# Kernel tuning notes

Hardware: AMD Instinct MI355X
Metric: run time of the kernel (lower is better)

## Reference

```python
import jax, jax.numpy as jnp
import numpy as np

AUDIO_DIM, SEM_DIM, ATTN_DIM = 512, 768, 128


def setup_inputs() -> dict:
    key = jax.random.key(0)
    ks = jax.random.split(key, 12)
    B, T, T_sem = 8, 4096, 1024
    s = lambda d: 1.0 / np.sqrt(d)
    return {
        "x_ct": jax.random.normal(ks[0], (B, AUDIO_DIM, T), jnp.float32),
        "sem_btd": jax.random.normal(ks[1], (B, T_sem, SEM_DIM), jnp.float32),
        "ln_w": jnp.ones((AUDIO_DIM,), jnp.float32),
        "ln_b": jnp.zeros((AUDIO_DIM,), jnp.float32),
        "Wq": jax.random.normal(ks[2], (AUDIO_DIM, ATTN_DIM), jnp.float32) * s(AUDIO_DIM),
        "bq": jnp.zeros((ATTN_DIM,), jnp.float32),
        "Wk": jax.random.normal(ks[3], (SEM_DIM, ATTN_DIM), jnp.float32) * s(SEM_DIM),
        "bk": jnp.zeros((ATTN_DIM,), jnp.float32),
        "Wv": jax.random.normal(ks[4], (SEM_DIM, ATTN_DIM), jnp.float32) * s(SEM_DIM),
        "bv": jnp.zeros((ATTN_DIM,), jnp.float32),
        "Wo": jax.random.normal(ks[5], (ATTN_DIM, AUDIO_DIM), jnp.float32) * s(ATTN_DIM),
        "bo": jnp.zeros((AUDIO_DIM,), jnp.float32),
    }


def _layernorm(x, w, b, eps=1e-5):
    mu = jnp.mean(x, axis=-1, keepdims=True)
    var = jnp.mean(jnp.square(x - mu), axis=-1, keepdims=True)
    return (x - mu) * jax.lax.rsqrt(var + eps) * w + b


def reference(x_ct, sem_btd, ln_w, ln_b, Wq, bq, Wk, bk, Wv, bv, Wo, bo):
    # x_ct: [B, C, T] -> [B, T, C]
    x = jnp.swapaxes(x_ct, 1, 2)
    x = _layernorm(x, ln_w, ln_b)
    Q = x @ Wq + bq                      # [B, T, A]
    K = sem_btd @ Wk + bk                # [B, S, A]
    V = sem_btd @ Wv + bv                # [B, S, A]
    scale = ATTN_DIM ** -0.5
    attn = jnp.einsum("bta,bsa->bts", Q, K) * scale
    attn = jax.nn.softmax(attn, axis=-1)  # dropout: eval mode (identity)
    ctx = jnp.einsum("bts,bsa->bta", attn, V)
    delta = ctx @ Wo + bo                # [B, T, C]
    return jnp.swapaxes(delta, 1, 2)     # [B, C, T]
```

## Files before the change

### kernel.cpp

```cpp
#include <hip/hip_runtime.h>
#include <hip/hip_bf16.h>
#include <math.h>

#define BATCH 8
#define TDIM 4096
#define SDIM 1024
#define CDIM 512
#define DDIM 768
#define ADIM 128

typedef short s8v __attribute__((ext_vector_type(8)));
typedef float f4v __attribute__((ext_vector_type(4)));

__device__ __forceinline__ short f2bf(float f) {
    unsigned u = __float_as_uint(f);
    u += 0x7fffu + ((u >> 16) & 1u);
    return (short)(u >> 16);
}
__device__ __forceinline__ float bf2f(short s) {
    return __uint_as_float(((unsigned)(unsigned short)s) << 16);
}
__device__ __forceinline__ f4v mfma16(s8v a, s8v b, f4v c) {
    return __builtin_amdgcn_mfma_f32_16x16x32_bf16(a, b, c, 0, 0, 0);
}

__global__ __launch_bounds__(256) void prep_w(
    const float* __restrict__ Wq, const float* __restrict__ Wk,
    const float* __restrict__ Wv, const float* __restrict__ Wo,
    const float* __restrict__ lnw, const float* __restrict__ lnb,
    short* __restrict__ WqT, short* __restrict__ WkT,
    short* __restrict__ WvT, short* __restrict__ WoT,
    float* __restrict__ uv)
{
    int tid = threadIdx.x;
    int gid = blockIdx.x * 256 + tid;
    {
        int k = gid >> 7, n = gid & 127;
        WqT[n * 512 + k] = f2bf(Wq[gid] * lnw[k]);
    }
    #pragma unroll
    for (int i = 0; i < 2; ++i) {
        int e = gid + i * 65536;
        if (e < 98304) {
            int k = e >> 7, n = e & 127;
            WkT[n * 768 + k] = f2bf(Wk[e]);
            WvT[n * 768 + k] = f2bf(Wv[e]);
        }
    }
    {
        int k = gid >> 9, c = gid & 511;
        WoT[c * 128 + k] = f2bf(Wo[gid]);
    }
    if (blockIdx.x < 32) {
        int a = tid & 127, half = tid >> 7;
        float pu = 0.f, pv = 0.f;
        #pragma unroll
        for (int cc = 0; cc < 8; ++cc) {
            int c = blockIdx.x * 16 + half * 8 + cc;
            float wq = Wq[c * 128 + a];
            pu += lnb[c] * wq;
            pv += lnw[c] * wq;
        }
        atomicAdd(&uv[a], pu);
        atomicAdd(&uv[128 + a], pv);
    }
}

__global__ __launch_bounds__(256) void kv_proj(
    const float* __restrict__ sem,
    const short* __restrict__ WkT, const float* __restrict__ bk,
    const short* __restrict__ WvT, const float* __restrict__ bv,
    short* __restrict__ Kb, short* __restrict__ Vb)
{
    __shared__ __align__(16) short sA[32 * 40];
    __shared__ __align__(16) short sW[2][128 * 40];
    const int tid = threadIdx.x, lane = tid & 63, wave = tid >> 6;
    const int ln15 = lane & 15, q = lane >> 4, kq = q * 8;
    const int r0 = blockIdx.x * 32;
    const int b = r0 >> 10, sbase = r0 & 1023;
    const int kv = wave >> 1;
    const int mh = wave & 1;
    const int m  = mh * 16 + ln15;

    f4v acc[8];
    #pragma unroll
    for (int j = 0; j < 8; ++j) acc[j] = (f4v)0.0f;

    const int srow = tid >> 3;
    const int sk4  = (tid & 7) * 4;

    for (int kc = 0; kc < DDIM / 32; ++kc) {
        __syncthreads();
        {
            float4 f = *(const float4*)&sem[(size_t)(r0 + srow) * DDIM + kc * 32 + sk4];
            uint2 pk;
            pk.x = (unsigned short)f2bf(f.x) | ((unsigned)(unsigned short)f2bf(f.y) << 16);
            pk.y = (unsigned short)f2bf(f.z) | ((unsigned)(unsigned short)f2bf(f.w) << 16);
            *(uint2*)&sA[srow * 40 + sk4] = pk;
        }
        #pragma unroll
        for (int i = 0; i < 2; ++i) {
            int idx8 = i * 256 + tid;
            int n = idx8 >> 2, k8 = (idx8 & 3) * 8;
            *(s8v*)&sW[0][n * 40 + k8] = *(const s8v*)&WkT[(size_t)n * 768 + kc * 32 + k8];
            *(s8v*)&sW[1][n * 40 + k8] = *(const s8v*)&WvT[(size_t)n * 768 + kc * 32 + k8];
        }
        __syncthreads();
        s8v a = *(const s8v*)&sA[m * 40 + kq];
        #pragma unroll
        for (int j = 0; j < 8; ++j) {
            s8v bb = *(const s8v*)&sW[kv][(j * 16 + ln15) * 40 + kq];
            acc[j] = mfma16(a, bb, acc[j]);
        }
    }
    const int s_in_b = sbase + mh * 16 + q * 4;
    if (kv == 0) {
        #pragma unroll
        for (int j = 0; j < 8; ++j) {
            int col = j * 16 + ln15;
            float bias = bk[col];
            #pragma unroll
            for (int r = 0; r < 4; ++r)
                Kb[((size_t)b * SDIM + s_in_b + r) * ADIM + col] = f2bf(acc[j][r] + bias);
        }
    } else {
        #pragma unroll
        for (int j = 0; j < 8; ++j) {
            int col = j * 16 + ln15;
            float bias = bv[col];
            uint2 pk;
            pk.x = (unsigned short)f2bf(acc[j][0] + bias) | ((unsigned)(unsigned short)f2bf(acc[j][1] + bias) << 16);
            pk.y = (unsigned short)f2bf(acc[j][2] + bias) | ((unsigned)(unsigned short)f2bf(acc[j][3] + bias) << 16);
            *(uint2*)&Vb[((size_t)b * ADIM + col) * SDIM + s_in_b] = pk;
        }
    }
}

__global__ __launch_bounds__(256) void ln_q(
    const float* __restrict__ x,
    const short* __restrict__ WqT,
    const float* __restrict__ bq,
    const float* __restrict__ uv,
    short* __restrict__ Qb)
{
    __shared__ __align__(16) short xt[32 * 512];
    __shared__ __align__(16) char  ubuf[128 * 76 * 2];
    __shared__ float smu[32], srs[32];
    short* sWq  = (short*)ubuf;
    float* red1 = (float*)ubuf;
    float* red2 = (float*)(ubuf + 4224);
    const int tid = threadIdx.x, lane = tid & 63, wave = tid >> 6;
    const int ln15 = lane & 15, q = lane >> 4, kq = q * 8;
    const int b = blockIdx.x >> 7;
    const int t0 = (blockIdx.x & 127) * 32;
    const float* xb = x + (size_t)b * CDIM * TDIM;

    const int tq  = (tid & 7) * 4;
    const int cb  = tid >> 3;
    const int rot = tid & 7;
    float ps1[4] = {0.f,0.f,0.f,0.f}, ps2[4] = {0.f,0.f,0.f,0.f};
    #pragma unroll
    for (int i = 0; i < 4; ++i) {
        float4 f[4];
        #pragma unroll
        for (int jc = 0; jc < 4; ++jc)
            f[jc] = *(const float4*)&xb[(size_t)(i * 128 + cb * 4 + jc) * TDIM + t0 + tq];
        const int c4 = i * 128 + cb * 4;
        const int blockX = ((c4 >> 3) ^ rot);
        const int offs = c4 & 7;
        #pragma unroll
        for (int jj = 0; jj < 4; ++jj) {
            float v0 = ((const float*)&f[0])[jj];
            float v1 = ((const float*)&f[1])[jj];
            float v2 = ((const float*)&f[2])[jj];
            float v3 = ((const float*)&f[3])[jj];
            ps1[jj] += (v0 + v1) + (v2 + v3);
            ps2[jj] += (v0*v0 + v1*v1) + (v2*v2 + v3*v3);
            uint2 pk;
            pk.x = (unsigned short)f2bf(v0) | ((unsigned)(unsigned short)f2bf(v1) << 16);
            pk.y = (unsigned short)f2bf(v2) | ((unsigned)(unsigned short)f2bf(v3) << 16);
            *(uint2*)&xt[(tq + jj) * 512 + blockX * 8 + offs] = pk;
        }
    }
    #pragma unroll
    for (int jj = 0; jj < 4; ++jj) {
        red1[(tq + jj) * 33 + cb] = ps1[jj];
        red2[(tq + jj) * 33 + cb] = ps2[jj];
    }
    __syncthreads();
    if (tid < 32) {
        float s1 = 0.f, s2 = 0.f;
        #pragma unroll 8
        for (int gg = 0; gg < 32; ++gg) { s1 += red1[tid * 33 + gg]; s2 += red2[tid * 33 + gg]; }
        float mu = s1 * (1.f / 512.f);
        float var = s2 * (1.f / 512.f) - mu * mu;
        smu[tid] = mu; srs[tid] = rsqrtf(var + 1e-5f);
    }

    f4v acc[4];
    #pragma unroll
    for (int j = 0; j < 4; ++j) acc[j] = (f4v)0.0f;
    const int mrow = (wave & 1) * 16 + ln15;
    const int jb = (wave >> 1) * 4;
    const int mr_rot = (mrow >> 2) & 7;
    s8v wreg[4];
    #pragma unroll
    for (int i = 0; i < 4; ++i) {
        int idx8 = i * 256 + tid;
        wreg[i] = *(const s8v*)&WqT[(size_t)(idx8 >> 3) * 512 + (idx8 & 7) * 8];
    }
    for (int kc = 0; kc < 8; ++kc) {
        __syncthreads();
        #pragma unroll
        for (int i = 0; i < 4; ++i) {
            int idx8 = i * 256 + tid;
            *(s8v*)&sWq[(idx8 >> 3) * 76 + (idx8 & 7) * 8] = wreg[i];
        }
        if (kc < 7) {
            #pragma unroll
            for (int i = 0; i < 4; ++i) {
                int idx8 = i * 256 + tid;
                wreg[i] = *(const s8v*)&WqT[(size_t)(idx8 >> 3) * 512 + (kc + 1) * 64 + (idx8 & 7) * 8];
            }
        }
        __syncthreads();
        #pragma unroll
        for (int kk = 0; kk < 2; ++kk) {
            int kb = kc * 8 + kk * 4 + q;
            s8v a = *(const s8v*)&xt[mrow * 512 + ((kb ^ mr_rot) << 3)];
            #pragma unroll
            for (int j = 0; j < 4; ++j) {
                s8v bb = *(const s8v*)&sWq[((jb + j) * 16 + ln15) * 76 + kk * 32 + kq];
                acc[j] = mfma16(a, bb, acc[j]);
            }
        }
    }
    const float scale = 0.08838834764831845f;
    #pragma unroll
    for (int j = 0; j < 4; ++j) {
        int col = (jb + j) * 16 + ln15;
        float uu = uv[col] + bq[col];
        float vv = uv[128 + col];
        #pragma unroll
        for (int r = 0; r < 4; ++r) {
            int tl = (wave & 1) * 16 + q * 4 + r;
            float qv = srs[tl] * acc[j][r] + uu - smu[tl] * srs[tl] * vv;
            Qb[((size_t)b * TDIM + t0 + tl) * ADIM + col] = f2bf(qv * scale);
        }
    }
}

__global__ __launch_bounds__(256) void attn(
    const short* __restrict__ Qb, const short* __restrict__ Kb,
    const short* __restrict__ Vb, short* __restrict__ Cx)
{
    __shared__ __align__(16) short sK [2][64 * 128];
    __shared__ __align__(16) short sVT[2][128 * 64];
    __shared__ __align__(16) short sP [64 * 64];
    const int tid = threadIdx.x, lane = tid & 63, wave = tid >> 6;
    const int ln15 = lane & 15, q = lane >> 4, kq = q * 8;
    const int b = blockIdx.x >> 6;
    const int t0 = (blockIdx.x & 63) * 64;
    const int m = wave * 16 + ln15;

    const int krow = tid >> 4, kkb = tid & 15;
    const int varow = tid >> 3, vkb = tid & 7;

    s8v qf[4];
    {
        const short* qp = Qb + ((size_t)b * TDIM + t0 + m) * ADIM + kq;
        #pragma unroll
        for (int kc = 0; kc < 4; ++kc) qf[kc] = *(const s8v*)(qp + kc * 32);
    }
    s8v ones;
    #pragma unroll
    for (int j = 0; j < 8; ++j) ones[j] = (short)0x3F80;

    f4v accO[8]; f4v accL = (f4v)0.0f;
    #pragma unroll
    for (int j = 0; j < 8; ++j) accO[j] = (f4v)0.0f;

    const short* Kbase = Kb + (size_t)b * SDIM * ADIM;
    const short* Vbase = Vb + (size_t)b * ADIM * SDIM;
    s8v rk[4], rv[4];

    #pragma unroll
    for (int i = 0; i < 4; ++i) {
        rk[i] = *(const s8v*)(Kbase + (size_t)(i * 16 + krow) * ADIM + kkb * 8);
        rv[i] = *(const s8v*)(Vbase + (size_t)(i * 32 + varow) * SDIM + vkb * 8);
    }
    #pragma unroll
    for (int i = 0; i < 4; ++i) {
        int r = i * 16 + krow;
        *(s8v*)&sK[0][r * 128 + ((kkb ^ (r & 15)) * 8)] = rk[i];
        int a = i * 32 + varow;
        *(s8v*)&sVT[0][a * 64 + ((vkb ^ (a & 7)) * 8)] = rv[i];
    }
    __syncthreads();

    for (int sc = 0; sc < SDIM / 64; ++sc) {
        const int cur = sc & 1;
        if (sc < 15) {
            const int s0n = (sc + 1) * 64;
            #pragma unroll
            for (int i = 0; i < 4; ++i) {
                rk[i] = *(const s8v*)(Kbase + (size_t)(s0n + i * 16 + krow) * ADIM + kkb * 8);
                rv[i] = *(const s8v*)(Vbase + (size_t)(i * 32 + varow) * SDIM + s0n + vkb * 8);
            }
        }
        #pragma unroll
        for (int j = 0; j < 4; ++j) {
            f4v sacc = (f4v)0.0f;
            const int row = j * 16 + ln15;
            #pragma unroll
            for (int kc = 0; kc < 4; ++kc) {
                s8v bb = *(const s8v*)&sK[cur][row * 128 + (((kc * 4 + q) ^ (row & 15)) * 8)];
                sacc = mfma16(qf[kc], bb, sacc);
            }
            #pragma unroll
            for (int r = 0; r < 4; ++r) {
                float ev = __expf(sacc[r]);
                int prow = wave * 16 + q * 4 + r;
                int pcol = j * 16 + ln15;
                sP[prow * 64 + (((pcol >> 3) ^ (prow & 7)) * 8) + (pcol & 7)] = f2bf(ev);
            }
        }
        #pragma unroll
        for (int kc = 0; kc < 2; ++kc) {
            s8v pa = *(const s8v*)&sP[m * 64 + (((kc * 4 + q) ^ (m & 7)) * 8)];
            accL = mfma16(pa, ones, accL);
            #pragma unroll
            for (int j = 0; j < 8; ++j) {
                int a = j * 16 + ln15;
                s8v bb = *(const s8v*)&sVT[cur][a * 64 + (((kc * 4 + q) ^ (a & 7)) * 8)];
                accO[j] = mfma16(pa, bb, accO[j]);
            }
        }
        if (sc < 15) {
            #pragma unroll
            for (int i = 0; i < 4; ++i) {
                int r = i * 16 + krow;
                *(s8v*)&sK[cur ^ 1][r * 128 + ((kkb ^ (r & 15)) * 8)] = rk[i];
                int a = i * 32 + varow;
                *(s8v*)&sVT[cur ^ 1][a * 64 + ((vkb ^ (a & 7)) * 8)] = rv[i];
            }
        }
        __syncthreads();
    }
    #pragma unroll
    for (int r = 0; r < 4; ++r) {
        float rinv = 1.0f / accL[r];
        int t = t0 + wave * 16 + q * 4 + r;
        #pragma unroll
        for (int j = 0; j < 8; ++j) {
            int col = j * 16 + ln15;
            Cx[((size_t)b * TDIM + t) * ADIM + col] = f2bf(accO[j][r] * rinv);
        }
    }
}

__global__ __launch_bounds__(256) void out_proj(
    const short* __restrict__ Cx, const short* __restrict__ WoT,
    const float* __restrict__ bo, float* __restrict__ out)
{
    __shared__ __align__(16) short sCtx[64 * 136];
    __shared__ __align__(16) char  buf[128 * 136 * 2];
    short* sWoT = (short*)buf;
    float* outT = (float*)buf;
    const int tid = threadIdx.x, lane = tid & 63, wave = tid >> 6;
    const int ln15 = lane & 15, q = lane >> 4, kq = q * 8;
    const int b = blockIdx.x >> 8;
    const int rem = blockIdx.x & 255;
    const int t0 = (rem & 63) * 64;
    const int c0 = (rem >> 6) * 128;

    #pragma unroll
    for (int i = 0; i < 4; ++i) {
        int idx8 = i * 256 + tid;
        int row = idx8 >> 4, a8 = (idx8 & 15) * 8;
        *(s8v*)&sCtx[row * 136 + a8] = *(const s8v*)&Cx[((size_t)b * TDIM + t0 + row) * ADIM + a8];
    }
    #pragma unroll
    for (int i = 0; i < 8; ++i) {
        int idx8 = i * 256 + tid;
        int n = idx8 >> 4, k8 = (idx8 & 15) * 8;
        *(s8v*)&sWoT[n * 136 + k8] = *(const s8v*)&WoT[(size_t)(c0 + n) * ADIM + k8];
    }
    __syncthreads();
    f4v acc[8];
    #pragma unroll
    for (int j = 0; j < 8; ++j) acc[j] = (f4v)0.0f;
    const int m = wave * 16 + ln15;
    #pragma unroll
    for (int kc = 0; kc < 4; ++kc) {
        s8v a = *(const s8v*)&sCtx[m * 136 + kc * 32 + kq];
        #pragma unroll
        for (int j = 0; j < 8; ++j) {
            s8v bb = *(const s8v*)&sWoT[(j * 16 + ln15) * 136 + kc * 32 + kq];
            acc[j] = mfma16(a, bb, acc[j]);
        }
    }
    __syncthreads();
    #pragma unroll
    for (int j = 0; j < 8; ++j) {
        int cl = j * 16 + ln15;
        float bias = bo[c0 + cl];
        #pragma unroll
        for (int r = 0; r < 4; ++r) {
            int tl = wave * 16 + q * 4 + r;
            outT[cl * 68 + tl] = acc[j][r] + bias;
        }
    }
    __syncthreads();
    #pragma unroll
    for (int i = 0; i < 8; ++i) {
        int idx4 = i * 256 + tid;
        int c = idx4 >> 4, t4 = (idx4 & 15) * 4;
        float4 v = *(const float4*)&outT[c * 68 + t4];
        *(float4*)&out[((size_t)b * CDIM + c0 + c) * TDIM + t0 + t4] = v;
    }
}

extern "C" void kernel_launch(void* const* d_in, const int* in_sizes, int n_in,
                              void* d_out, int out_size, void* d_ws, size_t ws_size,
                              hipStream_t stream) {
    const float* x   = (const float*)d_in[0];
    const float* sem = (const float*)d_in[1];
    const float* lnw = (const float*)d_in[2];
    const float* lnb = (const float*)d_in[3];
    const float* Wq  = (const float*)d_in[4];
    const float* bq  = (const float*)d_in[5];
    const float* Wk  = (const float*)d_in[6];
    const float* bk  = (const float*)d_in[7];
    const float* Wv  = (const float*)d_in[8];
    const float* bv  = (const float*)d_in[9];
    const float* Wo  = (const float*)d_in[10];
    const float* bo  = (const float*)d_in[11];
    float* out = (float*)d_out;

    short* ws  = (short*)d_ws;
    short* Qb  = ws;
    short* Kb  = Qb  + (size_t)BATCH * TDIM * ADIM;
    short* Vb  = Kb  + (size_t)BATCH * SDIM * ADIM;
    short* Cx  = Vb  + (size_t)BATCH * SDIM * ADIM;
    short* WqT = Cx  + (size_t)BATCH * TDIM * ADIM;
    short* WkT = WqT + 128 * 512;
    short* WvT = WkT + 128 * 768;
    short* WoT = WvT + 128 * 768;
    float* uv  = (float*)(WoT + 512 * 128);

    hipMemsetAsync(uv, 0, 256 * sizeof(float), stream);
    hipLaunchKernelGGL(prep_w,  dim3(256),  dim3(256), 0, stream,
                       Wq, Wk, Wv, Wo, lnw, lnb, WqT, WkT, WvT, WoT, uv);
    hipLaunchKernelGGL(kv_proj, dim3(256),  dim3(256), 0, stream, sem, WkT, bk, WvT, bv, Kb, Vb);
    hipLaunchKernelGGL(ln_q,    dim3(1024), dim3(256), 0, stream, x, WqT, bq, uv, Qb);
    hipLaunchKernelGGL(attn,    dim3(512),  dim3(256), 0, stream, Qb, Kb, Vb, Cx);
    hipLaunchKernelGGL(out_proj,dim3(2048), dim3(256), 0, stream, Cx, WoT, bo, out);
}
```

Before: 259.0 us.

## Read Wq fragments directly from global memory in LN+Q projection kernel

The LN+Q kernel no longer stages WqT through shared memory in eight chunks with paired barriers. Each wave now loads its B fragments straight from global/L2 and computes a 2x2 grid of 16x16 MFMA tiles over 32 output columns. The x transpose tile is rewritten to pack 8 channels per 16-byte store with a new XOR swizzle. This removes 16 block barriers and the shared-memory weight staging, at the cost of repeated uncoalesced-ish global weight reads across blocks.

```diff
diff --git a/kernel.cpp b/kernel.cpp
--- a/kernel.cpp
+++ b/kernel.cpp
@@ -16,9 +16,6 @@
     unsigned u = __float_as_uint(f);
     u += 0x7fffu + ((u >> 16) & 1u);
     return (short)(u >> 16);
-}
-__device__ __forceinline__ float bf2f(short s) {
-    return __uint_as_float(((unsigned)(unsigned short)s) << 16);
 }
 __device__ __forceinline__ f4v mfma16(s8v a, s8v b, f4v c) {
     return __builtin_amdgcn_mfma_f32_16x16x32_bf16(a, b, c, 0, 0, 0);
@@ -144,108 +141,92 @@
     short* __restrict__ Qb)
 {
     __shared__ __align__(16) short xt[32 * 512];
-    __shared__ __align__(16) char  ubuf[128 * 76 * 2];
+    __shared__ float red1[32][33], red2[32][33];
     __shared__ float smu[32], srs[32];
-    short* sWq  = (short*)ubuf;
-    float* red1 = (float*)ubuf;
-    float* red2 = (float*)(ubuf + 4224);
     const int tid = threadIdx.x, lane = tid & 63, wave = tid >> 6;
-    const int ln15 = lane & 15, q = lane >> 4, kq = q * 8;
+    const int ln15 = lane & 15, q = lane >> 4;
     const int b = blockIdx.x >> 7;
     const int t0 = (blockIdx.x & 127) * 32;
     const float* xb = x + (size_t)b * CDIM * TDIM;
 
-    const int tq  = (tid & 7) * 4;
-    const int cb  = tid >> 3;
-    const int rot = tid & 7;
+    const int tq = tid & 7;
+    const int cg = tid >> 3;
     float ps1[4] = {0.f,0.f,0.f,0.f}, ps2[4] = {0.f,0.f,0.f,0.f};
     #pragma unroll
-    for (int i = 0; i < 4; ++i) {
-        float4 f[4];
-        #pragma unroll
-        for (int jc = 0; jc < 4; ++jc)
-            f[jc] = *(const float4*)&xb[(size_t)(i * 128 + cb * 4 + jc) * TDIM + t0 + tq];
-        const int c4 = i * 128 + cb * 4;
-        const int blockX = ((c4 >> 3) ^ rot);
-        const int offs = c4 & 7;
+    for (int g8 = 0; g8 < 2; ++g8) {
+        float4 f[8];
+        #pragma unroll
+        for (int cc = 0; cc < 8; ++cc)
+            f[cc] = *(const float4*)&xb[(size_t)(cg * 16 + g8 * 8 + cc) * TDIM + t0 + tq * 4];
+        const int cb = cg * 2 + g8;
         #pragma unroll
         for (int jj = 0; jj < 4; ++jj) {
-            float v0 = ((const float*)&f[0])[jj];
-            float v1 = ((const float*)&f[1])[jj];
-            float v2 = ((const float*)&f[2])[jj];
-            float v3 = ((const float*)&f[3])[jj];
-            ps1[jj] += (v0 + v1) + (v2 + v3);
-            ps2[jj] += (v0*v0 + v1*v1) + (v2*v2 + v3*v3);
-            uint2 pk;
-            pk.x = (unsigned short)f2bf(v0) | ((unsigned)(unsigned short)f2bf(v1) << 16);
-            pk.y = (unsigned short)f2bf(v2) | ((unsigned)(unsigned short)f2bf(v3) << 16);
-            *(uint2*)&xt[(tq + jj) * 512 + blockX * 8 + offs] = pk;
+            const int t = tq * 4 + jj;
+            const int rot = ((t >> 1) ^ (t >> 3)) & 7;
+            s8v v;
+            #pragma unroll
+            for (int cc = 0; cc < 8; ++cc) {
+                float val = ((const float*)&f[cc])[jj];
+                ps1[jj] += val; ps2[jj] += val * val;
+                v[cc] = f2bf(val);
+            }
+            *(s8v*)&xt[t * 512 + ((cb ^ rot) * 8)] = v;
         }
     }
     #pragma unroll
     for (int jj = 0; jj < 4; ++jj) {
-        red1[(tq + jj) * 33 + cb] = ps1[jj];
-        red2[(tq + jj) * 33 + cb] = ps2[jj];
+        red1[tq * 4 + jj][cg] = ps1[jj];
+        red2[tq * 4 + jj][cg] = ps2[jj];
     }
     __syncthreads();
     if (tid < 32) {
         float s1 = 0.f, s2 = 0.f;
         #pragma unroll 8
-        for (int gg = 0; gg < 32; ++gg) { s1 += red1[tid * 33 + gg]; s2 += red2[tid * 33 + gg]; }
+        for (int g = 0; g < 32; ++g) { s1 += red1[tid][g]; s2 += red2[tid][g]; }
         float mu = s1 * (1.f / 512.f);
         float var = s2 * (1.f / 512.f) - mu * mu;
         smu[tid] = mu; srs[tid] = rsqrtf(var + 1e-5f);
     }
-
-    f4v acc[4];
-    #pragma unroll
-    for (int j = 0; j < 4; ++j) acc[j] = (f4v)0.0f;
-    const int mrow = (wave & 1) * 16 + ln15;
-    const int jb = (wave >> 1) * 4;
-    const int mr_rot = (mrow >> 2) & 7;
-    s8v wreg[4];
-    #pragma unroll
-    for (int i = 0; i < 4; ++i) {
-        int idx8 = i * 256 + tid;
-        wreg[i] = *(const s8v*)&WqT[(size_t)(idx8 >> 3) * 512 + (idx8 & 7) * 8];
-    }
-    for (int kc = 0; kc < 8; ++kc) {
-        __syncthreads();
-        #pragma unroll
-        for (int i = 0; i < 4; ++i) {
-            int idx8 = i * 256 + tid;
-            *(s8v*)&sWq[(idx8 >> 3) * 76 + (idx8 & 7) * 8] = wreg[i];
-        }
-        if (kc < 7) {
-            #pragma unroll
-            for (int i = 0; i < 4; ++i) {
-                int idx8 = i * 256 + tid;
-                wreg[i] = *(const s8v*)&WqT[(size_t)(idx8 >> 3) * 512 + (kc + 1) * 64 + (idx8 & 7) * 8];
-            }
-        }
-        __syncthreads();
-        #pragma unroll
-        for (int kk = 0; kk < 2; ++kk) {
-            int kb = kc * 8 + kk * 4 + q;
-            s8v a = *(const s8v*)&xt[mrow * 512 + ((kb ^ mr_rot) << 3)];
-            #pragma unroll
-            for (int j = 0; j < 4; ++j) {
-                s8v bb = *(const s8v*)&sWq[((jb + j) * 16 + ln15) * 76 + kk * 32 + kq];
-                acc[j] = mfma16(a, bb, acc[j]);
-            }
-        }
+    __syncthreads();
+
+    f4v acc[2][2];
+    #pragma unroll
+    for (int jm = 0; jm < 2; ++jm)
+        #pragma unroll
+        for (int jn = 0; jn < 2; ++jn) acc[jm][jn] = (f4v)0.0f;
+    const short* wp = WqT + (size_t)(wave * 32 + ln15) * 512 + q * 8;
+    #pragma unroll 4
+    for (int kk = 0; kk < 16; ++kk) {
+        s8v bfr[2], afr[2];
+        #pragma unroll
+        for (int jn = 0; jn < 2; ++jn)
+            bfr[jn] = *(const s8v*)(wp + jn * 16 * 512 + kk * 32);
+        #pragma unroll
+        for (int jm = 0; jm < 2; ++jm) {
+            const int t = jm * 16 + ln15;
+            const int rot = ((t >> 1) ^ (t >> 3)) & 7;
+            afr[jm] = *(const s8v*)&xt[t * 512 + (((kk * 4 + q) ^ rot) * 8)];
+        }
+        #pragma unroll
+        for (int jm = 0; jm < 2; ++jm)
+            #pragma unroll
+            for (int jn = 0; jn < 2; ++jn)
+                acc[jm][jn] = mfma16(afr[jm], bfr[jn], acc[jm][jn]);
     }
     const float scale = 0.08838834764831845f;
     #pragma unroll
-    for (int j = 0; j < 4; ++j) {
-        int col = (jb + j) * 16 + ln15;
-        float uu = uv[col] + bq[col];
-        float vv = uv[128 + col];
-        #pragma unroll
-        for (int r = 0; r < 4; ++r) {
-            int tl = (wave & 1) * 16 + q * 4 + r;
-            float qv = srs[tl] * acc[j][r] + uu - smu[tl] * srs[tl] * vv;
-            Qb[((size_t)b * TDIM + t0 + tl) * ADIM + col] = f2bf(qv * scale);
+    for (int jn = 0; jn < 2; ++jn) {
+        const int col = wave * 32 + jn * 16 + ln15;
+        const float uu = uv[col] + bq[col];
+        const float vv = uv[128 + col];
+        #pragma unroll
+        for (int jm = 0; jm < 2; ++jm) {
+            #pragma unroll
+            for (int r = 0; r < 4; ++r) {
+                const int tl = jm * 16 + q * 4 + r;
+                float qv = srs[tl] * acc[jm][jn][r] + uu - smu[tl] * srs[tl] * vv;
+                Qb[((size_t)b * TDIM + t0 + tl) * ADIM + col] = f2bf(qv * scale);
+            }
         }
     }
 }
```

Measured after the change: 241.7 us. 6.7% less time.
